# Performance work log

Measured on AMD Instinct MI355X. Metric: run time of the kernel, lower is better.

The kernel has to match this reference:

```python
import jax, jax.numpy as jnp
import numpy as np

SEQ_LEN, BATCH, IN_SIZE = 512, 1024, 3
HID, HID_FC, OUT = 512, 512, 1
HORIZON = 96


def gru_cell(x, h, w_ih, w_hh, b_ih, b_hh):
    # PyTorch GRU cell math. x: [B, in], h: [B, H], w_ih: [3H, in], w_hh: [3H, H]
    gi = x @ w_ih.T + b_ih
    gh = h @ w_hh.T + b_hh
    i_r, i_z, i_n = jnp.split(gi, 3, axis=-1)
    h_r, h_z, h_n = jnp.split(gh, 3, axis=-1)
    r = jax.nn.sigmoid(i_r + h_r)
    z = jax.nn.sigmoid(i_z + h_z)
    n = jnp.tanh(i_n + r * h_n)
    return (1.0 - z) * n + z * h


def setup_inputs() -> dict:
    key = jax.random.key(0)
    ks = jax.random.split(key, 16)
    s_in = 1.0 / np.sqrt(HID)
    inp = {
        'src': jax.random.normal(ks[0], (SEQ_LEN, BATCH, IN_SIZE), dtype=jnp.float32),
        'enc_wih': jax.random.uniform(ks[1], (3 * HID, IN_SIZE), minval=-s_in, maxval=s_in),
        'enc_whh': jax.random.uniform(ks[2], (3 * HID, HID), minval=-s_in, maxval=s_in),
        'enc_bih': jax.random.uniform(ks[3], (3 * HID,), minval=-s_in, maxval=s_in),
        'enc_bhh': jax.random.uniform(ks[4], (3 * HID,), minval=-s_in, maxval=s_in),
        'dec_wih': jax.random.uniform(ks[5], (3 * HID, OUT), minval=-s_in, maxval=s_in),
        'dec_whh': jax.random.uniform(ks[6], (3 * HID, HID), minval=-s_in, maxval=s_in),
        'dec_bih': jax.random.uniform(ks[7], (3 * HID,), minval=-s_in, maxval=s_in),
        'dec_bhh': jax.random.uniform(ks[8], (3 * HID,), minval=-s_in, maxval=s_in),
        'w1': jax.random.uniform(ks[9], (HID_FC, HID), minval=-s_in, maxval=s_in),
        'b1': jax.random.uniform(ks[10], (HID_FC,), minval=-s_in, maxval=s_in),
        'w2': jax.random.uniform(ks[11], (OUT, HID_FC), minval=-1.0 / np.sqrt(HID_FC), maxval=1.0 / np.sqrt(HID_FC)),
        'b2': jax.random.uniform(ks[12], (OUT,), minval=-1.0 / np.sqrt(HID_FC), maxval=1.0 / np.sqrt(HID_FC)),
        'horizon': HORIZON,
    }
    return inp


def reference(src, enc_wih, enc_whh, enc_bih, enc_bhh,
              dec_wih, dec_whh, dec_bih, dec_bhh,
              w1, b1, w2, b2, horizon):
    B = src.shape[1]
    h0 = jnp.zeros((B, HID), dtype=src.dtype)

    # Encoder: run GRU over time; only final hidden state is used.
    def enc_step(h, x_t):
        return gru_cell(x_t, h, enc_wih, enc_whh, enc_bih, enc_bhh), None
    h, _ = jax.lax.scan(enc_step, h0, src)

    dec_in0 = src[-1, :, 0:1]  # [B, 1]

    def dec_step(carry, _):
        dec_in, h = carry
        h = gru_cell(dec_in, h, dec_wih, dec_whh, dec_bih, dec_bhh)
        y = jax.nn.relu(h @ w1.T + b1) @ w2.T + b2  # [B, 1]
        return (y, h), y
    _, outputs = jax.lax.scan(dec_step, (dec_in0, h), None, length=horizon)
    return outputs  # [horizon, B, 1]
```

## Files before the change

### kernel.cpp

```cpp
#include <hip/hip_runtime.h>

typedef __bf16 bf16x8 __attribute__((ext_vector_type(8)));
typedef float f32x4 __attribute__((ext_vector_type(4)));

#define HID 512
#define BATCH 1024
#define SEQL 512
#define NWG 256
#define NTHR 256

#define OFF_ENH 0u
#define OFF_ENL 1572864u
#define OFF_DEH 3145728u
#define OFF_DEL 4718592u
#define OFF_W1H 6291456u
#define OFF_W1L 6815744u
#define OFF_HP0 7340032u
#define OFF_HP1 9437184u
#define OFF_FC1 11534336u
#define OFF_BAR 13631488u
#define WS_NEED 13635584u

#define LDS_LO 32768
#define SWZ(row, cb) (((row) << 9) + ((cb) ^ (((row) & 7) << 4)))

__device__ __forceinline__ f32x4 mfma16(bf16x8 a, bf16x8 b, f32x4 c) {
  return __builtin_amdgcn_mfma_f32_16x16x32_bf16(a, b, c, 0, 0, 0);
}
__device__ __forceinline__ float sig_(float x) { return 1.0f / (1.0f + __expf(-x)); }
__device__ __forceinline__ float tanh_(float x) { return 1.0f - 2.0f / (__expf(2.0f * x) + 1.0f); }

__device__ __forceinline__ unsigned long long ald64(const void* p) {
  return __hip_atomic_load((const unsigned long long*)p, __ATOMIC_RELAXED,
                           __HIP_MEMORY_SCOPE_AGENT);
}
__device__ __forceinline__ void ast32(void* p, unsigned v) {
  __hip_atomic_store((unsigned*)p, v, __ATOMIC_RELAXED, __HIP_MEMORY_SCOPE_AGENT);
}
__device__ __forceinline__ void astf(void* p, float v) {
  __hip_atomic_store((float*)p, v, __ATOMIC_RELAXED, __HIP_MEMORY_SCOPE_AGENT);
}

__global__ void split_w(const float* __restrict__ a, __bf16* __restrict__ hi,
                        __bf16* __restrict__ lo, int n) {
  int i = blockIdx.x * blockDim.x + threadIdx.x;
  if (i < n) {
    float v = a[i];
    __bf16 h = (__bf16)v;
    hi[i] = h;
    lo[i] = (__bf16)(v - (float)h);
  }
}

__device__ __forceinline__ void gbar(unsigned* cnt, unsigned target) {
  __syncthreads();
  if (threadIdx.x == 0) {
    __hip_atomic_fetch_add(cnt, 1u, __ATOMIC_RELAXED, __HIP_MEMORY_SCOPE_AGENT);
    int i = 0;
    while (__hip_atomic_load(cnt, __ATOMIC_RELAXED, __HIP_MEMORY_SCOPE_AGENT) < target) {
      __builtin_amdgcn_s_sleep(2);
      if (++i >= 20000) break;
    }
  }
  __syncthreads();
  __builtin_amdgcn_sched_barrier(0);
}

__device__ __forceinline__ void stage_half(char* sm, const unsigned* hsrc, int row0,
                                           int khalf, int tid) {
  const int cp = tid & 127;
  const int rh = (tid >> 7) << 5;
  const unsigned long long* src = (const unsigned long long*)hsrc +
                                  ((size_t)(row0 + rh) << 8) + (khalf << 7) + cp;
  unsigned long long b0[16], b1[16];
#pragma unroll
  for (int j = 0; j < 16; ++j) b0[j] = ald64(src + (size_t)j * 256);
#pragma unroll
  for (int j = 0; j < 16; ++j) b1[j] = ald64(src + (size_t)(16 + j) * 256);
  auto PR = [&](unsigned long long(&b)[16], int r0) {
#pragma unroll
    for (int j = 0; j < 16; ++j) {
      const int row = rh + r0 + j;
      const unsigned p0 = (unsigned)b[j];
      const unsigned p1 = (unsigned)(b[j] >> 32);
      const unsigned hw = (p0 & 0xffffu) | (p1 << 16);
      const unsigned lw = (p0 >> 16) | (p1 & 0xffff0000u);
      const int sa = SWZ(row, cp << 2);
      *(unsigned*)(sm + sa) = hw;
      *(unsigned*)(sm + LDS_LO + sa) = lw;
    }
  };
  PR(b0, 0);
  PR(b1, 16);
}

__device__ __forceinline__ void gh6h(const char* sm, int rl, int kbb, int khalf,
                                     const __bf16* __restrict__ Bh,
                                     const __bf16* __restrict__ Bl,
                                     const int (&boff)[6], f32x4 (&acc)[6]) {
#pragma unroll 4
  for (int kc = 0; kc < 8; ++kc) {
    const int sa = SWZ(rl, (kc << 6) + kbb);
    bf16x8 ah = *(const bf16x8*)(sm + sa);
    bf16x8 al = *(const bf16x8*)(sm + LDS_LO + sa);
    const int ko = (khalf << 8) + (kc << 5);
#pragma unroll
    for (int f = 0; f < 6; ++f) {
      bf16x8 bh = *(const bf16x8*)(Bh + boff[f] + ko);
      bf16x8 bl = *(const bf16x8*)(Bl + boff[f] + ko);
      acc[f] = mfma16(ah, bh, acc[f]);
      acc[f] = mfma16(al, bh, acc[f]);
      acc[f] = mfma16(ah, bl, acc[f]);
    }
  }
}

__device__ __forceinline__ void gh2h(const char* sm, int rl, int kbb, int khalf,
                                     const __bf16* __restrict__ Bh,
                                     const __bf16* __restrict__ Bl,
                                     const int (&boff)[2], f32x4 (&acc)[2]) {
#pragma unroll 4
  for (int kc = 0; kc < 8; ++kc) {
    const int sa = SWZ(rl, (kc << 6) + kbb);
    bf16x8 ah = *(const bf16x8*)(sm + sa);
    bf16x8 al = *(const bf16x8*)(sm + LDS_LO + sa);
    const int ko = (khalf << 8) + (kc << 5);
#pragma unroll
    for (int f = 0; f < 2; ++f) {
      bf16x8 bh = *(const bf16x8*)(Bh + boff[f] + ko);
      bf16x8 bl = *(const bf16x8*)(Bl + boff[f] + ko);
      acc[f] = mfma16(ah, bh, acc[f]);
      acc[f] = mfma16(al, bh, acc[f]);
      acc[f] = mfma16(ah, bl, acc[f]);
    }
  }
}

__global__ void __launch_bounds__(NTHR, 1) seq2seq_main(
    const float* __restrict__ src, const float* __restrict__ enc_wih,
    const float* __restrict__ enc_bih, const float* __restrict__ enc_bhh,
    const float* __restrict__ dec_wih, const float* __restrict__ dec_bih,
    const float* __restrict__ dec_bhh, const float* __restrict__ b1,
    const float* __restrict__ w2, const float* __restrict__ b2,
    const int* __restrict__ hor, float* __restrict__ out, char* __restrict__ ws) {
  __shared__ f32x4 smv[4096];
  char* sm = (char*)smv;
  float* yb = (float*)sm;

  const __bf16* ench_hi = (const __bf16*)(ws + OFF_ENH);
  const __bf16* ench_lo = (const __bf16*)(ws + OFF_ENL);
  const __bf16* dech_hi = (const __bf16*)(ws + OFF_DEH);
  const __bf16* dech_lo = (const __bf16*)(ws + OFF_DEL);
  const __bf16* w1h = (const __bf16*)(ws + OFF_W1H);
  const __bf16* w1l = (const __bf16*)(ws + OFF_W1L);
  unsigned* hp0 = (unsigned*)(ws + OFF_HP0);
  unsigned* hp1 = (unsigned*)(ws + OFF_HP1);
  float* fc1 = (float*)(ws + OFF_FC1);

  const int bid = blockIdx.x;
  const int g = (bid & 7) + ((bid >> 7) << 3);
  const int ct = (bid >> 3) & 15;
  const int tid = threadIdx.x;
  const int wv = tid >> 6;
  const int lane = tid & 63;
  const int lan15 = lane & 15;
  const int crow = (lane >> 4) << 2;
  const int kbe = (lane >> 4) << 3;
  const int kbb = kbe << 1;
  const int rl = (wv << 4) + lan15;
  const int row0 = g << 6;

  unsigned* cnt = (unsigned*)(ws + OFF_BAR) + (g << 6);

  int boff[6];
#pragma unroll
  for (int gg = 0; gg < 3; ++gg)
#pragma unroll
    for (int ch = 0; ch < 2; ++ch)
      boff[gg * 2 + ch] = ((gg << 9) + (ct << 5) + (ch << 4) + lan15) * HID + kbe;
  int bofffc[2];
#pragma unroll
  for (int ch = 0; ch < 2; ++ch) bofffc[ch] = ((ct << 5) + (ch << 4) + lan15) * HID + kbe;

  float wE[2][3][3], biE[2][3], bhE[2][3];
#pragma unroll
  for (int ch = 0; ch < 2; ++ch)
#pragma unroll
    for (int gg = 0; gg < 3; ++gg) {
      const int j = (gg << 9) + (ct << 5) + (ch << 4) + lan15;
      wE[ch][gg][0] = enc_wih[j * 3 + 0];
      wE[ch][gg][1] = enc_wih[j * 3 + 1];
      wE[ch][gg][2] = enc_wih[j * 3 + 2];
      biE[ch][gg] = enc_bih[j];
      bhE[ch][gg] = enc_bhh[j];
    }

  const f32x4 zf = {0.0f, 0.0f, 0.0f, 0.0f};
  float hpv[2][4] = {{0.f, 0.f, 0.f, 0.f}, {0.f, 0.f, 0.f, 0.f}};

  for (int t = 0; t < SEQL; ++t) {
    f32x4 acc[6];
#pragma unroll
    for (int f = 0; f < 6; ++f) acc[f] = zf;

    if (t != 0) {
      const unsigned* hsrc = (t & 1) ? hp1 : hp0;
      stage_half(sm, hsrc, row0, 0, tid);
      __syncthreads();
      gh6h(sm, rl, kbb, 0, ench_hi, ench_lo, boff, acc);
      __syncthreads();
      stage_half(sm, hsrc, row0, 1, tid);
      __syncthreads();
      gh6h(sm, rl, kbb, 1, ench_hi, ench_lo, boff, acc);
    }

    unsigned* hn = ((t + 1) & 1) ? hp1 : hp0;
#pragma unroll
    for (int reg = 0; reg < 4; ++reg) {
      const int row = row0 + (wv << 4) + crow + reg;
      const float* xp = src + ((size_t)t * BATCH + row) * 3;
      const float x0 = xp[0], x1 = xp[1], x2 = xp[2];
#pragma unroll
      for (int ch = 0; ch < 2; ++ch) {
        const float gir =
            fmaf(x0, wE[ch][0][0], fmaf(x1, wE[ch][0][1], fmaf(x2, wE[ch][0][2], biE[ch][0])));
        const float giz =
            fmaf(x0, wE[ch][1][0], fmaf(x1, wE[ch][1][1], fmaf(x2, wE[ch][1][2], biE[ch][1])));
        const float gin =
            fmaf(x0, wE[ch][2][0], fmaf(x1, wE[ch][2][1], fmaf(x2, wE[ch][2][2], biE[ch][2])));
        const float rg = sig_(gir + acc[ch][reg] + bhE[ch][0]);
        const float zg = sig_(giz + acc[2 + ch][reg] + bhE[ch][1]);
        const float ng = tanh_(gin + rg * (acc[4 + ch][reg] + bhE[ch][2]));
        const float hv = fmaf(zg, hpv[ch][reg] - ng, ng);
        hpv[ch][reg] = hv;
        const __bf16 hb = (__bf16)hv;
        const __bf16 lb = (__bf16)(hv - (float)hb);
        const unsigned pw = (unsigned)__builtin_bit_cast(unsigned short, hb) |
                            ((unsigned)__builtin_bit_cast(unsigned short, lb) << 16);
        ast32(hn + (size_t)row * HID + (ct << 5) + (ch << 4) + lan15, pw);
      }
    }
    gbar(cnt, 16u * (unsigned)(t + 1));
  }

  float wD[2][3], biD[2][3], bhD[2][3], b1c[2];
#pragma unroll
  for (int ch = 0; ch < 2; ++ch) {
#pragma unroll
    for (int gg = 0; gg < 3; ++gg) {
      const int j = (gg << 9) + (ct << 5) + (ch << 4) + lan15;
      wD[ch][gg] = dec_wih[j];
      biD[ch][gg] = dec_bih[j];
      bhD[ch][gg] = dec_bhh[j];
    }
    b1c[ch] = b1[(ct << 5) + (ch << 4) + lan15];
  }
  const float b2v = b2[0];
  float w2p0[4], w2p1[4];
#pragma unroll
  for (int j = 0; j < 4; ++j) {
    w2p0[j] = w2[2 * (lane + j * 64)];
    w2p1[j] = w2[2 * (lane + j * 64) + 1];
  }
  int H = hor[0];
  if (H < 1 || H > 96) H = 96;

  for (int t = 0; t < H; ++t) {
    float din[4];
    if (t == 0) {
#pragma unroll
      for (int reg = 0; reg < 4; ++reg) {
        const int row = row0 + (wv << 4) + crow + reg;
        din[reg] = src[((size_t)(SEQL - 1) * BATCH + row) * 3];
      }
    } else {
#pragma unroll 2
      for (int rr = 0; rr < 16; ++rr) {
        const int row = row0 + (wv << 4) + rr;
        const unsigned long long* fp = (const unsigned long long*)fc1 + ((size_t)row << 8);
        float s = 0.0f;
#pragma unroll
        for (int j = 0; j < 4; ++j) {
          const unsigned long long w = ald64(fp + lane + (j << 6));
          const float f0 = __builtin_bit_cast(float, (unsigned)(w & 0xffffffffULL));
          const float f1 = __builtin_bit_cast(float, (unsigned)(w >> 32));
          s = fmaf(f0, w2p0[j], fmaf(f1, w2p1[j], s));
        }
#pragma unroll
        for (int off = 1; off < 64; off <<= 1) s += __shfl_xor(s, off, 64);
        if (lane == 0) yb[(wv << 4) + rr] = s + b2v;
      }
      __syncthreads();
      if (ct == 0 && tid < 64) out[(size_t)(t - 1) * BATCH + row0 + tid] = yb[tid];
#pragma unroll
      for (int reg = 0; reg < 4; ++reg) din[reg] = yb[(wv << 4) + crow + reg];
      __syncthreads();
    }

    {
      const unsigned* hsrc = (t & 1) ? hp1 : hp0;
      f32x4 acc[6];
#pragma unroll
      for (int f = 0; f < 6; ++f) acc[f] = zf;
      stage_half(sm, hsrc, row0, 0, tid);
      __syncthreads();
      gh6h(sm, rl, kbb, 0, dech_hi, dech_lo, boff, acc);
      __syncthreads();
      stage_half(sm, hsrc, row0, 1, tid);
      __syncthreads();
      gh6h(sm, rl, kbb, 1, dech_hi, dech_lo, boff, acc);

      unsigned* hn = ((t + 1) & 1) ? hp1 : hp0;
#pragma unroll
      for (int reg = 0; reg < 4; ++reg) {
        const int row = row0 + (wv << 4) + crow + reg;
        const float d = din[reg];
#pragma unroll
        for (int ch = 0; ch < 2; ++ch) {
          const float rg = sig_(fmaf(d, wD[ch][0], biD[ch][0]) + acc[ch][reg] + bhD[ch][0]);
          const float zg = sig_(fmaf(d, wD[ch][1], biD[ch][1]) + acc[2 + ch][reg] + bhD[ch][1]);
          const float ng =
              tanh_(fmaf(d, wD[ch][2], biD[ch][2]) + rg * (acc[4 + ch][reg] + bhD[ch][2]));
          const float hv = fmaf(zg, hpv[ch][reg] - ng, ng);
          hpv[ch][reg] = hv;
          const __bf16 hb = (__bf16)hv;
          const __bf16 lb = (__bf16)(hv - (float)hb);
          const unsigned pw = (unsigned)__builtin_bit_cast(unsigned short, hb) |
                              ((unsigned)__builtin_bit_cast(unsigned short, lb) << 16);
          ast32(hn + (size_t)row * HID + (ct << 5) + (ch << 4) + lan15, pw);
        }
      }
    }
    gbar(cnt, 16u * (unsigned)(SEQL + 2 * t + 1));

    {
      const unsigned* hsrc = ((t + 1) & 1) ? hp1 : hp0;
      f32x4 fa[2];
      fa[0] = zf;
      fa[1] = zf;
      stage_half(sm, hsrc, row0, 0, tid);
      __syncthreads();
      gh2h(sm, rl, kbb, 0, w1h, w1l, bofffc, fa);
      __syncthreads();
      stage_half(sm, hsrc, row0, 1, tid);
      __syncthreads();
      gh2h(sm, rl, kbb, 1, w1h, w1l, bofffc, fa);
#pragma unroll
      for (int reg = 0; reg < 4; ++reg) {
        const int row = row0 + (wv << 4) + crow + reg;
#pragma unroll
        for (int ch = 0; ch < 2; ++ch) {
          astf(&fc1[(size_t)row * HID + (ct << 5) + (ch << 4) + lan15],
               fmaxf(fa[ch][reg] + b1c[ch], 0.0f));
        }
      }
    }
    gbar(cnt, 16u * (unsigned)(SEQL + 2 * t + 2));
  }

  if (ct == 0) {
#pragma unroll 2
    for (int rr = 0; rr < 16; ++rr) {
      const int row = row0 + (wv << 4) + rr;
      const unsigned long long* fp = (const unsigned long long*)fc1 + ((size_t)row << 8);
      float s = 0.0f;
#pragma unroll
      for (int j = 0; j < 4; ++j) {
        const unsigned long long w = ald64(fp + lane + (j << 6));
        const float f0 = __builtin_bit_cast(float, (unsigned)(w & 0xffffffffULL));
        const float f1 = __builtin_bit_cast(float, (unsigned)(w >> 32));
        s = fmaf(f0, w2p0[j], fmaf(f1, w2p1[j], s));
      }
#pragma unroll
      for (int off = 1; off < 64; off <<= 1) s += __shfl_xor(s, off, 64);
      if (lane == 0) yb[(wv << 4) + rr] = s + b2v;
    }
    __syncthreads();
    if (tid < 64) out[(size_t)(H - 1) * BATCH + row0 + tid] = yb[tid];
  }
}

extern "C" void kernel_launch(void* const* d_in, const int* in_sizes, int n_in,
                              void* d_out, int out_size, void* d_ws, size_t ws_size,
                              hipStream_t stream) {
  if (ws_size < WS_NEED) return;

  const float* src = (const float*)d_in[0];
  const float* enc_wih = (const float*)d_in[1];
  const float* enc_whh = (const float*)d_in[2];
  const float* enc_bih = (const float*)d_in[3];
  const float* enc_bhh = (const float*)d_in[4];
  const float* dec_wih = (const float*)d_in[5];
  const float* dec_whh = (const float*)d_in[6];
  const float* dec_bih = (const float*)d_in[7];
  const float* dec_bhh = (const float*)d_in[8];
  const float* w1 = (const float*)d_in[9];
  const float* b1 = (const float*)d_in[10];
  const float* w2 = (const float*)d_in[11];
  const float* b2 = (const float*)d_in[12];
  const int* hor = (const int*)d_in[13];
  float* out = (float*)d_out;
  char* ws = (char*)d_ws;

  hipMemsetAsync(ws + OFF_BAR, 0, 4096, stream);

  split_w<<<dim3(3072), dim3(256), 0, stream>>>(enc_whh, (__bf16*)(ws + OFF_ENH),
                                                (__bf16*)(ws + OFF_ENL), 786432);
  split_w<<<dim3(3072), dim3(256), 0, stream>>>(dec_whh, (__bf16*)(ws + OFF_DEH),
                                                (__bf16*)(ws + OFF_DEL), 786432);
  split_w<<<dim3(1024), dim3(256), 0, stream>>>(w1, (__bf16*)(ws + OFF_W1H),
                                                (__bf16*)(ws + OFF_W1L), 262144);

  void* args[] = {&src, &enc_wih, &enc_bih, &enc_bhh, &dec_wih, &dec_bih, &dec_bhh,
                  &b1, &w2, &b2, &hor, &out, &ws};
  hipLaunchCooperativeKernel((void*)seq2seq_main, dim3(NWG), dim3(NTHR), args, 0, stream);
}
```

Before: 18.34 ms.

## Repartition GRU work into 32-row groups with 512-thread blocks and single-pass staging

Changes the work split so each workgroup owns 32 batch rows and 64 hidden columns with 8 waves, instead of 64 rows and 32 columns with 4 waves. Barrier groups shrink from 16 to 8 workgroups. The full 512-wide hidden state is staged into LDS in one pass rather than two halves, which drops two __syncthreads per GEMM phase. The intent is to cut per-step latency in the serial recurrence through smaller barrier groups and fewer syncs. In exchange each wave does less MFMA work per weight fetch, and the 512-thread blocks raise register pressure.

```diff
diff --git a/kernel.cpp b/kernel.cpp
--- a/kernel.cpp
+++ b/kernel.cpp
@@ -7,7 +7,7 @@
 #define BATCH 1024
 #define SEQL 512
 #define NWG 256
-#define NTHR 256
+#define NTHR 512
 
 #define OFF_ENH 0u
 #define OFF_ENL 1572864u
@@ -22,7 +22,7 @@
 #define WS_NEED 13635584u
 
 #define LDS_LO 32768
-#define SWZ(row, cb) (((row) << 9) + ((cb) ^ (((row) & 7) << 4)))
+#define SWZ(row, cb) (((row) << 10) + ((cb) ^ (((row) & 7) << 4)))
 
 __device__ __forceinline__ f32x4 mfma16(bf16x8 a, bf16x8 b, f32x4 c) {
   return __builtin_amdgcn_mfma_f32_16x16x32_bf16(a, b, c, 0, 0, 0);
@@ -59,53 +59,46 @@
     int i = 0;
     while (__hip_atomic_load(cnt, __ATOMIC_RELAXED, __HIP_MEMORY_SCOPE_AGENT) < target) {
       __builtin_amdgcn_s_sleep(2);
-      if (++i >= 20000) break;
+      if (++i >= 30000) break;
     }
   }
   __syncthreads();
   __builtin_amdgcn_sched_barrier(0);
 }
 
-__device__ __forceinline__ void stage_half(char* sm, const unsigned* hsrc, int row0,
-                                           int khalf, int tid) {
-  const int cp = tid & 127;
-  const int rh = (tid >> 7) << 5;
-  const unsigned long long* src = (const unsigned long long*)hsrc +
-                                  ((size_t)(row0 + rh) << 8) + (khalf << 7) + cp;
-  unsigned long long b0[16], b1[16];
-#pragma unroll
-  for (int j = 0; j < 16; ++j) b0[j] = ald64(src + (size_t)j * 256);
-#pragma unroll
-  for (int j = 0; j < 16; ++j) b1[j] = ald64(src + (size_t)(16 + j) * 256);
-  auto PR = [&](unsigned long long(&b)[16], int r0) {
-#pragma unroll
-    for (int j = 0; j < 16; ++j) {
-      const int row = rh + r0 + j;
-      const unsigned p0 = (unsigned)b[j];
-      const unsigned p1 = (unsigned)(b[j] >> 32);
-      const unsigned hw = (p0 & 0xffffu) | (p1 << 16);
-      const unsigned lw = (p0 >> 16) | (p1 & 0xffff0000u);
-      const int sa = SWZ(row, cp << 2);
-      *(unsigned*)(sm + sa) = hw;
-      *(unsigned*)(sm + LDS_LO + sa) = lw;
-    }
-  };
-  PR(b0, 0);
-  PR(b1, 16);
-}
-
-__device__ __forceinline__ void gh6h(const char* sm, int rl, int kbb, int khalf,
-                                     const __bf16* __restrict__ Bh,
-                                     const __bf16* __restrict__ Bl,
-                                     const int (&boff)[6], f32x4 (&acc)[6]) {
+__device__ __forceinline__ void stage_h32(char* sm, const unsigned* hsrc, int row0, int tid) {
+  const int cp = tid & 255;
+  const int rh = (tid >> 8) << 4;
+  const unsigned long long* src =
+      (const unsigned long long*)hsrc + ((size_t)(row0 + rh) << 8) + cp;
+  unsigned long long b[16];
+#pragma unroll
+  for (int j = 0; j < 16; ++j) b[j] = ald64(src + (size_t)j * 256);
+#pragma unroll
+  for (int j = 0; j < 16; ++j) {
+    const int row = rh + j;
+    const unsigned p0 = (unsigned)b[j];
+    const unsigned p1 = (unsigned)(b[j] >> 32);
+    const unsigned hw = (p0 & 0xffffu) | (p1 << 16);
+    const unsigned lw = (p0 >> 16) | (p1 & 0xffff0000u);
+    const int sa = SWZ(row, cp << 2);
+    *(unsigned*)(sm + sa) = hw;
+    *(unsigned*)(sm + LDS_LO + sa) = lw;
+  }
+}
+
+__device__ __forceinline__ void gh3(const char* sm, int rl, int kbb,
+                                    const __bf16* __restrict__ Bh,
+                                    const __bf16* __restrict__ Bl,
+                                    const int (&boff)[3], f32x4 (&acc)[3]) {
 #pragma unroll 4
-  for (int kc = 0; kc < 8; ++kc) {
+  for (int kc = 0; kc < 16; ++kc) {
     const int sa = SWZ(rl, (kc << 6) + kbb);
     bf16x8 ah = *(const bf16x8*)(sm + sa);
     bf16x8 al = *(const bf16x8*)(sm + LDS_LO + sa);
-    const int ko = (khalf << 8) + (kc << 5);
-#pragma unroll
-    for (int f = 0; f < 6; ++f) {
+    const int ko = kc << 5;
+#pragma unroll
+    for (int f = 0; f < 3; ++f) {
       bf16x8 bh = *(const bf16x8*)(Bh + boff[f] + ko);
       bf16x8 bl = *(const bf16x8*)(Bl + boff[f] + ko);
       acc[f] = mfma16(ah, bh, acc[f]);
@@ -115,28 +108,24 @@
   }
 }
 
-__device__ __forceinline__ void gh2h(const char* sm, int rl, int kbb, int khalf,
-                                     const __bf16* __restrict__ Bh,
-                                     const __bf16* __restrict__ Bl,
-                                     const int (&boff)[2], f32x4 (&acc)[2]) {
+__device__ __forceinline__ void gh1(const char* sm, int rl, int kbb,
+                                    const __bf16* __restrict__ Bh,
+                                    const __bf16* __restrict__ Bl, int boff, f32x4& acc) {
 #pragma unroll 4
-  for (int kc = 0; kc < 8; ++kc) {
+  for (int kc = 0; kc < 16; ++kc) {
     const int sa = SWZ(rl, (kc << 6) + kbb);
     bf16x8 ah = *(const bf16x8*)(sm + sa);
     bf16x8 al = *(const bf16x8*)(sm + LDS_LO + sa);
-    const int ko = (khalf << 8) + (kc << 5);
-#pragma unroll
-    for (int f = 0; f < 2; ++f) {
-      bf16x8 bh = *(const bf16x8*)(Bh + boff[f] + ko);
-      bf16x8 bl = *(const bf16x8*)(Bl + boff[f] + ko);
-      acc[f] = mfma16(ah, bh, acc[f]);
-      acc[f] = mfma16(al, bh, acc[f]);
-      acc[f] = mfma16(ah, bl, acc[f]);
-    }
-  }
-}
-
-__global__ void __launch_bounds__(NTHR, 1) seq2seq_main(
+    const int ko = kc << 5;
+    bf16x8 bh = *(const bf16x8*)(Bh + boff + ko);
+    bf16x8 bl = *(const bf16x8*)(Bl + boff + ko);
+    acc = mfma16(ah, bh, acc);
+    acc = mfma16(al, bh, acc);
+    acc = mfma16(ah, bl, acc);
+  }
+}
+
+__global__ void __launch_bounds__(NTHR, 2) seq2seq_main(
     const float* __restrict__ src, const float* __restrict__ enc_wih,
     const float* __restrict__ enc_bih, const float* __restrict__ enc_bhh,
     const float* __restrict__ dec_wih, const float* __restrict__ dec_bih,
@@ -158,8 +147,8 @@
   float* fc1 = (float*)(ws + OFF_FC1);
 
   const int bid = blockIdx.x;
-  const int g = (bid & 7) + ((bid >> 7) << 3);
-  const int ct = (bid >> 3) & 15;
+  const int G = bid >> 3;
+  const int ct = bid & 7;
   const int tid = threadIdx.x;
   const int wv = tid >> 6;
   const int lane = tid & 63;
@@ -167,94 +156,76 @@
   const int crow = (lane >> 4) << 2;
   const int kbe = (lane >> 4) << 3;
   const int kbb = kbe << 1;
-  const int rl = (wv << 4) + lan15;
-  const int row0 = g << 6;
-
-  unsigned* cnt = (unsigned*)(ws + OFF_BAR) + (g << 6);
-
-  int boff[6];
-#pragma unroll
-  for (int gg = 0; gg < 3; ++gg)
-#pragma unroll
-    for (int ch = 0; ch < 2; ++ch)
-      boff[gg * 2 + ch] = ((gg << 9) + (ct << 5) + (ch << 4) + lan15) * HID + kbe;
-  int bofffc[2];
-#pragma unroll
-  for (int ch = 0; ch < 2; ++ch) bofffc[ch] = ((ct << 5) + (ch << 4) + lan15) * HID + kbe;
-
-  float wE[2][3][3], biE[2][3], bhE[2][3];
-#pragma unroll
-  for (int ch = 0; ch < 2; ++ch)
-#pragma unroll
-    for (int gg = 0; gg < 3; ++gg) {
-      const int j = (gg << 9) + (ct << 5) + (ch << 4) + lan15;
-      wE[ch][gg][0] = enc_wih[j * 3 + 0];
-      wE[ch][gg][1] = enc_wih[j * 3 + 1];
-      wE[ch][gg][2] = enc_wih[j * 3 + 2];
-      biE[ch][gg] = enc_bih[j];
-      bhE[ch][gg] = enc_bhh[j];
-    }
+  const int wr = wv & 1;
+  const int wc = wv >> 1;
+  const int rl = (wr << 4) + lan15;
+  const int row0 = G << 5;
+  const int cg = (ct << 6) + (wc << 4) + lan15;
+
+  unsigned* cnt = (unsigned*)(ws + OFF_BAR) + (G << 5);
+
+  int boff[3];
+#pragma unroll
+  for (int g = 0; g < 3; ++g) boff[g] = ((g << 9) + cg) * HID + kbe;
+  const int boff_fc = cg * HID + kbe;
+
+  float wE[3][3], biE[3], bhE[3];
+#pragma unroll
+  for (int g = 0; g < 3; ++g) {
+    const int j = (g << 9) + cg;
+    wE[g][0] = enc_wih[j * 3 + 0];
+    wE[g][1] = enc_wih[j * 3 + 1];
+    wE[g][2] = enc_wih[j * 3 + 2];
+    biE[g] = enc_bih[j];
+    bhE[g] = enc_bhh[j];
+  }
 
   const f32x4 zf = {0.0f, 0.0f, 0.0f, 0.0f};
-  float hpv[2][4] = {{0.f, 0.f, 0.f, 0.f}, {0.f, 0.f, 0.f, 0.f}};
+  float hpv[4] = {0.f, 0.f, 0.f, 0.f};
 
   for (int t = 0; t < SEQL; ++t) {
-    f32x4 acc[6];
-#pragma unroll
-    for (int f = 0; f < 6; ++f) acc[f] = zf;
+    f32x4 acc[3];
+#pragma unroll
+    for (int f = 0; f < 3; ++f) acc[f] = zf;
 
     if (t != 0) {
-      const unsigned* hsrc = (t & 1) ? hp1 : hp0;
-      stage_half(sm, hsrc, row0, 0, tid);
-      __syncthreads();
-      gh6h(sm, rl, kbb, 0, ench_hi, ench_lo, boff, acc);
-      __syncthreads();
-      stage_half(sm, hsrc, row0, 1, tid);
-      __syncthreads();
-      gh6h(sm, rl, kbb, 1, ench_hi, ench_lo, boff, acc);
+      stage_h32(sm, (t & 1) ? hp1 : hp0, row0, tid);
+      __syncthreads();
+      gh3(sm, rl, kbb, ench_hi, ench_lo, boff, acc);
     }
 
     unsigned* hn = ((t + 1) & 1) ? hp1 : hp0;
 #pragma unroll
     for (int reg = 0; reg < 4; ++reg) {
-      const int row = row0 + (wv << 4) + crow + reg;
+      const int row = row0 + (wr << 4) + crow + reg;
       const float* xp = src + ((size_t)t * BATCH + row) * 3;
       const float x0 = xp[0], x1 = xp[1], x2 = xp[2];
-#pragma unroll
-      for (int ch = 0; ch < 2; ++ch) {
-        const float gir =
-            fmaf(x0, wE[ch][0][0], fmaf(x1, wE[ch][0][1], fmaf(x2, wE[ch][0][2], biE[ch][0])));
-        const float giz =
-            fmaf(x0, wE[ch][1][0], fmaf(x1, wE[ch][1][1], fmaf(x2, wE[ch][1][2], biE[ch][1])));
-        const float gin =
-            fmaf(x0, wE[ch][2][0], fmaf(x1, wE[ch][2][1], fmaf(x2, wE[ch][2][2], biE[ch][2])));
-        const float rg = sig_(gir + acc[ch][reg] + bhE[ch][0]);
-        const float zg = sig_(giz + acc[2 + ch][reg] + bhE[ch][1]);
-        const float ng = tanh_(gin + rg * (acc[4 + ch][reg] + bhE[ch][2]));
-        const float hv = fmaf(zg, hpv[ch][reg] - ng, ng);
-        hpv[ch][reg] = hv;
-        const __bf16 hb = (__bf16)hv;
-        const __bf16 lb = (__bf16)(hv - (float)hb);
-        const unsigned pw = (unsigned)__builtin_bit_cast(unsigned short, hb) |
-                            ((unsigned)__builtin_bit_cast(unsigned short, lb) << 16);
-        ast32(hn + (size_t)row * HID + (ct << 5) + (ch << 4) + lan15, pw);
-      }
-    }
-    gbar(cnt, 16u * (unsigned)(t + 1));
-  }
-
-  float wD[2][3], biD[2][3], bhD[2][3], b1c[2];
-#pragma unroll
-  for (int ch = 0; ch < 2; ++ch) {
-#pragma unroll
-    for (int gg = 0; gg < 3; ++gg) {
-      const int j = (gg << 9) + (ct << 5) + (ch << 4) + lan15;
-      wD[ch][gg] = dec_wih[j];
-      biD[ch][gg] = dec_bih[j];
-      bhD[ch][gg] = dec_bhh[j];
-    }
-    b1c[ch] = b1[(ct << 5) + (ch << 4) + lan15];
-  }
+      const float gir = fmaf(x0, wE[0][0], fmaf(x1, wE[0][1], fmaf(x2, wE[0][2], biE[0])));
+      const float giz = fmaf(x0, wE[1][0], fmaf(x1, wE[1][1], fmaf(x2, wE[1][2], biE[1])));
+      const float gin = fmaf(x0, wE[2][0], fmaf(x1, wE[2][1], fmaf(x2, wE[2][2], biE[2])));
+      const float rg = sig_(gir + acc[0][reg] + bhE[0]);
+      const float zg = sig_(giz + acc[1][reg] + bhE[1]);
+      const float ng = tanh_(gin + rg * (acc[2][reg] + bhE[2]));
+      const float hv = fmaf(zg, hpv[reg] - ng, ng);
+      hpv[reg] = hv;
+      const __bf16 hb = (__bf16)hv;
+      const __bf16 lb = (__bf16)(hv - (float)hb);
+      const unsigned pw = (unsigned)__builtin_bit_cast(unsigned short, hb) |
+                          ((unsigned)__builtin_bit_cast(unsigned short, lb) << 16);
+      ast32(hn + (size_t)row * HID + cg, pw);
+    }
+    gbar(cnt, 8u * (unsigned)(t + 1));
+  }
+
+  float wD[3], biD[3], bhD[3];
+#pragma unroll
+  for (int g = 0; g < 3; ++g) {
+    const int j = (g << 9) + cg;
+    wD[g] = dec_wih[j];
+    biD[g] = dec_bih[j];
+    bhD[g] = dec_bhh[j];
+  }
+  const float b1c = b1[cg];
   const float b2v = b2[0];
   float w2p0[4], w2p1[4];
 #pragma unroll
@@ -270,13 +241,13 @@
     if (t == 0) {
 #pragma unroll
       for (int reg = 0; reg < 4; ++reg) {
-        const int row = row0 + (wv << 4) + crow + reg;
+        const int row = row0 + (wr << 4) + crow + reg;
         din[reg] = src[((size_t)(SEQL - 1) * BATCH + row) * 3];
       }
     } else {
-#pragma unroll 2
-      for (int rr = 0; rr < 16; ++rr) {
-        const int row = row0 + (wv << 4) + rr;
+#pragma unroll
+      for (int rr = 0; rr < 4; ++rr) {
+        const int row = row0 + (wv << 2) + rr;
         const unsigned long long* fp = (const unsigned long long*)fc1 + ((size_t)row << 8);
         float s = 0.0f;
 #pragma unroll
@@ -288,80 +259,60 @@
         }
 #pragma unroll
         for (int off = 1; off < 64; off <<= 1) s += __shfl_xor(s, off, 64);
-        if (lane == 0) yb[(wv << 4) + rr] = s + b2v;
-      }
-      __syncthreads();
-      if (ct == 0 && tid < 64) out[(size_t)(t - 1) * BATCH + row0 + tid] = yb[tid];
-#pragma unroll
-      for (int reg = 0; reg < 4; ++reg) din[reg] = yb[(wv << 4) + crow + reg];
+        if (lane == 0) yb[(wv << 2) + rr] = s + b2v;
+      }
+      __syncthreads();
+      if (ct == 0 && tid < 32) out[(size_t)(t - 1) * BATCH + row0 + tid] = yb[tid];
+#pragma unroll
+      for (int reg = 0; reg < 4; ++reg) din[reg] = yb[(wr << 4) + crow + reg];
       __syncthreads();
     }
 
     {
-      const unsigned* hsrc = (t & 1) ? hp1 : hp0;
-      f32x4 acc[6];
-#pragma unroll
-      for (int f = 0; f < 6; ++f) acc[f] = zf;
-      stage_half(sm, hsrc, row0, 0, tid);
-      __syncthreads();
-      gh6h(sm, rl, kbb, 0, dech_hi, dech_lo, boff, acc);
-      __syncthreads();
-      stage_half(sm, hsrc, row0, 1, tid);
-      __syncthreads();
-      gh6h(sm, rl, kbb, 1, dech_hi, dech_lo, boff, acc);
+      stage_h32(sm, (t & 1) ? hp1 : hp0, row0, tid);
+      __syncthreads();
+      f32x4 acc[3];
+#pragma unroll
+      for (int f = 0; f < 3; ++f) acc[f] = zf;
+      gh3(sm, rl, kbb, dech_hi, dech_lo, boff, acc);
 
       unsigned* hn = ((t + 1) & 1) ? hp1 : hp0;
 #pragma unroll
       for (int reg = 0; reg < 4; ++reg) {
-        const int row = row0 + (wv << 4) + crow + reg;
+        const int row = row0 + (wr << 4) + crow + reg;
         const float d = din[reg];
-#pragma unroll
-        for (int ch = 0; ch < 2; ++ch) {
-          const float rg = sig_(fmaf(d, wD[ch][0], biD[ch][0]) + acc[ch][reg] + bhD[ch][0]);
-          const float zg = sig_(fmaf(d, wD[ch][1], biD[ch][1]) + acc[2 + ch][reg] + bhD[ch][1]);
-          const float ng =
-              tanh_(fmaf(d, wD[ch][2], biD[ch][2]) + rg * (acc[4 + ch][reg] + bhD[ch][2]));
-          const float hv = fmaf(zg, hpv[ch][reg] - ng, ng);
-          hpv[ch][reg] = hv;
-          const __bf16 hb = (__bf16)hv;
-          const __bf16 lb = (__bf16)(hv - (float)hb);
-          const unsigned pw = (unsigned)__builtin_bit_cast(unsigned short, hb) |
-                              ((unsigned)__builtin_bit_cast(unsigned short, lb) << 16);
-          ast32(hn + (size_t)row * HID + (ct << 5) + (ch << 4) + lan15, pw);
-        }
-      }
-    }
-    gbar(cnt, 16u * (unsigned)(SEQL + 2 * t + 1));
+        const float rg = sig_(fmaf(d, wD[0], biD[0]) + acc[0][reg] + bhD[0]);
+        const float zg = sig_(fmaf(d, wD[1], biD[1]) + acc[1][reg] + bhD[1]);
+        const float ng = tanh_(fmaf(d, wD[2], biD[2]) + rg * (acc[2][reg] + bhD[2]));
+        const float hv = fmaf(zg, hpv[reg] - ng, ng);
+        hpv[reg] = hv;
+        const __bf16 hb = (__bf16)hv;
+        const __bf16 lb = (__bf16)(hv - (float)hb);
+        const unsigned pw = (unsigned)__builtin_bit_cast(unsigned short, hb) |
+                            ((unsigned)__builtin_bit_cast(unsigned short, lb) << 16);
+        ast32(hn + (size_t)row * HID + cg, pw);
+      }
+    }
+    gbar(cnt, 8u * (unsigned)(SEQL + 2 * t + 1));
 
     {
-      const unsigned* hsrc = ((t + 1) & 1) ? hp1 : hp0;
-      f32x4 fa[2];
-      fa[0] = zf;
-      fa[1] = zf;
-      stage_half(sm, hsrc, row0, 0, tid);
-      __syncthreads();
-      gh2h(sm, rl, kbb, 0, w1h, w1l, bofffc, fa);
-      __syncthreads();
-      stage_half(sm, hsrc, row0, 1, tid);
-      __syncthreads();
-      gh2h(sm, rl, kbb, 1, w1h, w1l, bofffc, fa);
+      stage_h32(sm, ((t + 1) & 1) ? hp1 : hp0, row0, tid);
+      __syncthreads();
+      f32x4 fa = zf;
+      gh1(sm, rl, kbb, w1h, w1l, boff_fc, fa);
 #pragma unroll
       for (int reg = 0; reg < 4; ++reg) {
-        const int row = row0 + (wv << 4) + crow + reg;
-#pragma unroll
-        for (int ch = 0; ch < 2; ++ch) {
-          astf(&fc1[(size_t)row * HID + (ct << 5) + (ch << 4) + lan15],
-               fmaxf(fa[ch][reg] + b1c[ch], 0.0f));
-        }
-      }
-    }
-    gbar(cnt, 16u * (unsigned)(SEQL + 2 * t + 2));
+        const int row = row0 + (wr << 4) + crow + reg;
+        astf(&fc1[(size_t)row * HID + cg], fmaxf(fa[reg] + b1c, 0.0f));
+      }
+    }
+    gbar(cnt, 8u * (unsigned)(SEQL + 2 * t + 2));
   }
 
   if (ct == 0) {
-#pragma unroll 2
-    for (int rr = 0; rr < 16; ++rr) {
-      const int row = row0 + (wv << 4) + rr;
+#pragma unroll
+    for (int rr = 0; rr < 4; ++rr) {
+      const int row = row0 + (wv << 2) + rr;
       const unsigned long long* fp = (const unsigned long long*)fc1 + ((size_t)row << 8);
       float s = 0.0f;
 #pragma unroll
@@ -373,10 +324,10 @@
       }
 #pragma unroll
       for (int off = 1; off < 64; off <<= 1) s += __shfl_xor(s, off, 64);
-      if (lane == 0) yb[(wv << 4) + rr] = s + b2v;
+      if (lane == 0) yb[(wv << 2) + rr] = s + b2v;
     }
     __syncthreads();
-    if (tid < 64) out[(size_t)(H - 1) * BATCH + row0 + tid] = yb[tid];
+    if (tid < 32) out[(size_t)(H - 1) * BATCH + row0 + tid] = yb[tid];
   }
 }
 
```

Result: faster. 16.29 ms (-11.1%).
